# Kernel tuning notes

Measured on AMD Instinct MI355X. Metric: run time of the kernel, lower is better.

The kernel has to match this reference:

```python
import jax, jax.numpy as jnp
import numpy as np

DIM = 1024
NUM_HEADS = 16
HEAD_DIM = DIM // NUM_HEADS
EPS = 1e-5


def layernorm(x, scale, bias):
    # LayerNorm over the last (head_dim) axis
    mu = jnp.mean(x, axis=-1, keepdims=True)
    var = jnp.var(x, axis=-1, keepdims=True)
    return (x - mu) * jax.lax.rsqrt(var + EPS) * scale + bias


def rope(q):
    # q: [B, H, S, Hd]; standard rotate-half RoPE over head_dim
    S, Hd = q.shape[-2], q.shape[-1]
    inv_freq = 1.0 / (10000.0 ** (jnp.arange(0, Hd, 2, dtype=jnp.float32) / Hd))
    ang = jnp.arange(S, dtype=jnp.float32)[:, None] * inv_freq  # [S, Hd/2]
    cos, sin = jnp.cos(ang), jnp.sin(ang)
    q1, q2 = jnp.split(q, 2, axis=-1)
    return jnp.concatenate([q1 * cos - q2 * sin, q1 * sin + q2 * cos], axis=-1)


def setup_inputs() -> dict:
    key = jax.random.key(0)
    ks = jax.random.split(key, 8)
    B, S, S_ctx = 4, 2048, 2048
    s = 0.02
    return {
        "x": jax.random.normal(ks[0], (B, S, DIM), dtype=jnp.float32),
        "context": jax.random.normal(ks[1], (B, S_ctx, DIM), dtype=jnp.float32),
        "q_w": jax.random.normal(ks[2], (DIM, DIM), dtype=jnp.float32) * s,
        "kv_w": jax.random.normal(ks[3], (DIM, 2 * DIM), dtype=jnp.float32) * s,
        "qn_scale": jnp.ones((HEAD_DIM,), jnp.float32),
        "qn_bias": jnp.zeros((HEAD_DIM,), jnp.float32),
        "kn_scale": jnp.ones((HEAD_DIM,), jnp.float32),
        "kn_bias": jnp.zeros((HEAD_DIM,), jnp.float32),
        "proj_w": jax.random.normal(ks[4], (DIM, DIM), dtype=jnp.float32) * s,
        "proj_b": jnp.zeros((DIM,), jnp.float32),
    }


def reference(x, context, q_w, kv_w, qn_scale, qn_bias, kn_scale, kn_bias, proj_w, proj_b):
    B, S, C = x.shape
    S_ctx = context.shape[1]
    H, Hd = NUM_HEADS, HEAD_DIM
    # projections (no bias: qkv_bias=False)
    q = (x @ q_w).reshape(B, S, H, Hd).transpose(0, 2, 1, 3)        # [B,H,S,Hd]
    kv = (context @ kv_w).reshape(B, S_ctx, 2, H, Hd)
    k = kv[:, :, 0].transpose(0, 2, 1, 3)                           # [B,H,Sc,Hd]
    v = kv[:, :, 1].transpose(0, 2, 1, 3)
    # per-head LayerNorm on q and k
    q = layernorm(q, qn_scale, qn_bias)
    k = layernorm(k, kn_scale, kn_bias)
    # RoPE on q only (as in the original forward)
    q = rope(q)
    # SDPA (eval path: no mask, no dropout)
    scale = 1.0 / jnp.sqrt(jnp.float32(Hd))
    logits = jnp.einsum("bhsd,bhtd->bhst", q, k) * scale
    attn = jax.nn.softmax(logits, axis=-1)
    out = jnp.einsum("bhst,bhtd->bhsd", attn, v)                    # [B,H,S,Hd]
    out = out.transpose(0, 2, 1, 3).reshape(B, S, C)
    return out @ proj_w + proj_b
```

## Files before the change

kernel.cpp:

```cpp
#include <hip/hip_runtime.h>
#include <hip/hip_bf16.h>


typedef short bf16x8 __attribute__((ext_vector_type(8)));
typedef float f32x4 __attribute__((ext_vector_type(4)));

__device__ __forceinline__ short f2s(float f) {
    __hip_bfloat16 h = __float2bfloat16(f);
    return __builtin_bit_cast(short, h);
}

__device__ __forceinline__ f32x4 mfma16(bf16x8 a, bf16x8 b, f32x4 c) {
    return __builtin_amdgcn_mfma_f32_16x16x32_bf16(a, b, c, 0, 0, 0);
}

__device__ __forceinline__ void gload16(short* lds, const short* g) {
    __builtin_amdgcn_global_load_lds((const __attribute__((address_space(1))) void*)g,
                                     (__attribute__((address_space(3))) void*)lds,
                                     16, 0, 0);
}

__device__ __forceinline__ void drain_barrier() {
    asm volatile("s_waitcnt vmcnt(0) lgkmcnt(0)" ::: "memory");
    __syncthreads();
}

__device__ __forceinline__ unsigned int fbits(float f) {
    return __builtin_bit_cast(unsigned int, f);
}

__global__ __launch_bounds__(256) void conv_to_bf16(const float* __restrict__ x,
                                                    const float* __restrict__ ctx,
                                                    short* __restrict__ xb,
                                                    short* __restrict__ cb) {
    const size_t NV = 2097152;
    size_t i = (size_t)blockIdx.x * 256 + threadIdx.x;
    const float4* src = (i < NV) ? (const float4*)x : (const float4*)ctx;
    short* dst = (i < NV) ? xb : cb;
    size_t idx = (i < NV) ? i : i - NV;
    float4 v = src[idx];
    short4 o;
    o.x = f2s(v.x); o.y = f2s(v.y); o.z = f2s(v.z); o.w = f2s(v.w);
    ((short4*)dst)[idx] = o;
}

__global__ __launch_bounds__(256) void transpose_weights(
    const float* __restrict__ q_w, const float* __restrict__ kv_w,
    const float* __restrict__ proj_w,
    short* __restrict__ WqT, short* __restrict__ WkvT, short* __restrict__ WpT) {
    __shared__ float t[32][33];
    const float* src; short* dst; int ld, coff;
    switch (blockIdx.z) {
        case 0:  src = q_w;    dst = WqT;                 ld = 1024; coff = 0;    break;
        case 1:  src = kv_w;   dst = WkvT;                ld = 2048; coff = 0;    break;
        case 2:  src = kv_w;   dst = WkvT + 1024 * 1024;  ld = 2048; coff = 1024; break;
        default: src = proj_w; dst = WpT;                 ld = 1024; coff = 0;    break;
    }
    int n0 = blockIdx.x * 32, k0 = blockIdx.y * 32;
    int tx = threadIdx.x & 31, ty = threadIdx.x >> 5;
    #pragma unroll
    for (int j = 0; j < 32; j += 8)
        t[ty + j][tx] = src[(size_t)(k0 + ty + j) * ld + coff + n0 + tx];
    __syncthreads();
    #pragma unroll
    for (int j = 0; j < 32; j += 8)
        dst[(size_t)(n0 + ty + j) * 1024 + k0 + tx] = f2s(t[tx][ty + j]);
}

template <int MODE>
__global__ __launch_bounds__(256) void gemm128(
    const short* __restrict__ A,
    const short* __restrict__ Bt,
    const float* __restrict__ ln_scale,
    const float* __restrict__ ln_bias,
    short* __restrict__ outB,
    short* __restrict__ outB2,
    float* __restrict__ outF,
    const float* __restrict__ bias_vec) {
    __shared__ short smem[24576];
    const int tid = threadIdx.x;
    const int w = tid >> 6, lane = tid & 63, quad = lane >> 4, l15 = lane & 15;
    const int wr = w & 1, wc = w >> 1;
    const int m0 = blockIdx.y * 128, n0 = blockIdx.x * 128;

    const int srow = lane >> 2, slot = lane & 3;
    const int kslot = (slot ^ ((srow >> 1) & 3)) * 8;
    const short* Ag0 = A + (size_t)(m0 + w * 32 + srow) * 1024 + kslot;
    const short* Ag1 = Ag0 + (size_t)16 * 1024;
    const short* Bg0 = Bt + (size_t)(n0 + w * 32 + srow) * 1024 + kslot;
    const short* Bg1 = Bg0 + (size_t)16 * 1024;
    short* Al = smem + w * 1024;
    short* Bl = smem + 4096 + w * 1024;

    f32x4 acc[4][4];
    #pragma unroll
    for (int r = 0; r < 4; r++)
        #pragma unroll
        for (int c = 0; c < 4; c++) acc[r][c] = f32x4{0.f, 0.f, 0.f, 0.f};

    const int rsw = (l15 >> 1) & 3;
    const int rch = (quad ^ rsw) * 8;

    gload16(Al,              Ag0);
    gload16(Al + 512,        Ag1);
    gload16(Bl,              Bg0);
    gload16(Bl + 512,        Bg1);
    gload16(Al + 8192,       Ag0 + 32);
    gload16(Al + 8192 + 512, Ag1 + 32);
    gload16(Bl + 8192,       Bg0 + 32);
    gload16(Bl + 8192 + 512, Bg1 + 32);
    asm volatile("s_waitcnt vmcnt(4) lgkmcnt(0)" ::: "memory");
    __builtin_amdgcn_s_barrier();

    int curo = 0;
    int pfo = 16384;
    #pragma unroll 1
    for (int t = 0; t < 32; t++) {
        if (t < 30) {
            const int k0 = (t + 2) * 32;
            gload16(Al + pfo,       Ag0 + k0);
            gload16(Al + pfo + 512, Ag1 + k0);
            gload16(Bl + pfo,       Bg0 + k0);
            gload16(Bl + pfo + 512, Bg1 + k0);
        }
        bf16x8 af[4], bfr[4];
        #pragma unroll
        for (int rt = 0; rt < 4; rt++)
            af[rt] = *(const bf16x8*)(smem + curo + (wr * 64 + rt * 16 + l15) * 32 + rch);
        #pragma unroll
        for (int ct = 0; ct < 4; ct++)
            bfr[ct] = *(const bf16x8*)(smem + curo + 4096 + (wc * 64 + ct * 16 + l15) * 32 + rch);
        #pragma unroll
        for (int rt = 0; rt < 4; rt++)
            #pragma unroll
            for (int ct = 0; ct < 4; ct++)
                acc[rt][ct] = mfma16(af[rt], bfr[ct], acc[rt][ct]);
        if (t < 30) {
            asm volatile("s_waitcnt vmcnt(4) lgkmcnt(0)" ::: "memory");
        } else {
            asm volatile("s_waitcnt vmcnt(0) lgkmcnt(0)" ::: "memory");
        }
        __builtin_amdgcn_s_barrier();
        curo += 8192; if (curo == 24576) curo = 0;
        pfo  += 8192; if (pfo  == 24576) pfo  = 0;
    }

    const bool vpath = (MODE == 1) && (n0 >= 1024);
    if constexpr (MODE == 0 || MODE == 1) {
        if (!vpath) {
            #pragma unroll
            for (int rt = 0; rt < 4; rt++) {
                #pragma unroll
                for (int i = 0; i < 4; i++) {
                    float s = acc[rt][0][i] + acc[rt][1][i] + acc[rt][2][i] + acc[rt][3][i];
                    float q = acc[rt][0][i] * acc[rt][0][i] + acc[rt][1][i] * acc[rt][1][i] +
                              acc[rt][2][i] * acc[rt][2][i] + acc[rt][3][i] * acc[rt][3][i];
                    #pragma unroll
                    for (int off = 1; off < 16; off <<= 1) {
                        s += __shfl_xor(s, off, 64);
                        q += __shfl_xor(q, off, 64);
                    }
                    float mu = s * (1.f / 64.f);
                    float var = q * (1.f / 64.f) - mu * mu;
                    float rs = rsqrtf(var + 1e-5f);
                    float vals[4];
                    #pragma unroll
                    for (int ct = 0; ct < 4; ct++) {
                        int hd = ct * 16 + l15;
                        vals[ct] = (acc[rt][ct][i] - mu) * rs * ln_scale[hd] + ln_bias[hd];
                    }
                    if constexpr (MODE == 0) {
                        int sp = (m0 + wr * 64 + rt * 16 + quad * 4 + i) & 2047;
                        #pragma unroll
                        for (int ct = 0; ct < 2; ct++) {
                            int hd1 = ct * 16 + l15;
                            float ang = (float)sp * exp2f((float)hd1 * (-13.287712379549449f / 32.f));
                            float sn, cs;
                            sincosf(ang, &sn, &cs);
                            float v1 = vals[ct], v2 = vals[ct + 2];
                            vals[ct]     = v1 * cs - v2 * sn;
                            vals[ct + 2] = v1 * sn + v2 * cs;
                        }
                        #pragma unroll
                        for (int ct = 0; ct < 4; ct++) vals[ct] *= 0.1803368801f;
                    }
                    #pragma unroll
                    for (int ct = 0; ct < 4; ct++) acc[rt][ct][i] = vals[ct];
                }
            }
            drain_barrier();
            short* Csm = smem;
            #pragma unroll
            for (int rt = 0; rt < 4; rt++)
                #pragma unroll
                for (int ct = 0; ct < 4; ct++)
                    #pragma unroll
                    for (int i = 0; i < 4; i++)
                        Csm[(wr * 64 + rt * 16 + quad * 4 + i) * 132 + wc * 64 + ct * 16 + l15] =
                            f2s(acc[rt][ct][i]);
            drain_barrier();
            #pragma unroll
            for (int it = 0; it < 8; it++) {
                int row = it * 16 + (tid >> 4);
                int chunk = tid & 15;
                bf16x8 v = *(const bf16x8*)(Csm + row * 132 + chunk * 8);
                int hh = ((n0 & 1023) >> 6) + (chunk >> 3);
                int m = m0 + row, b = m >> 11, sp = m & 2047;
                *(bf16x8*)(outB + ((size_t)(b * 16 + hh) * 2048 + sp) * 64 + (chunk & 7) * 8) = v;
            }
        } else {
            const int b = m0 >> 11, h = ((n0 - 1024) >> 6) + wc;
            const int sp = (m0 & 2047) + wr * 64 + quad * 4;
            #pragma unroll
            for (int rt = 0; rt < 4; rt++)
                #pragma unroll
                for (int ct = 0; ct < 4; ct++) {
                    short4 pk;
                    pk.x = f2s(acc[rt][ct][0]); pk.y = f2s(acc[rt][ct][1]);
                    pk.z = f2s(acc[rt][ct][2]); pk.w = f2s(acc[rt][ct][3]);
                    int hd = ct * 16 + l15;
                    *(short4*)(outB2 + ((size_t)(b * 16 + h) * 64 + hd) * 2048 + sp + rt * 16) = pk;
                }
        }
    } else {
        #pragma unroll
        for (int rt = 0; rt < 4; rt++)
            #pragma unroll
            for (int i = 0; i < 4; i++) {
                size_t m = m0 + wr * 64 + rt * 16 + quad * 4 + i;
                #pragma unroll
                for (int ct = 0; ct < 4; ct++) {
                    int n = n0 + wc * 64 + ct * 16 + l15;
                    outF[m * 1024 + n] = acc[rt][ct][i] + bias_vec[n];
                }
            }
    }
}

__global__ __launch_bounds__(256, 2) void attn_kernel(
    const short* __restrict__ Q,
    const short* __restrict__ K,
    const short* __restrict__ V,
    short* __restrict__ AO) {
    __shared__ short smem[8192 + 8192 + 2 * 4 * 32 * 72];
    const int tid = threadIdx.x;
    const int w = tid >> 6, lane = tid & 63, quad = lane >> 4, l15 = lane & 15;
    const int bh = blockIdx.x, qt = blockIdx.y;
    const short* Qb = Q + (size_t)bh * 2048 * 64;
    const short* Kb = K + (size_t)bh * 2048 * 64;
    const short* Vb = V + (size_t)bh * 64 * 2048;
    const int q0g[2] = {qt * 128 + w * 32, (qt + 8) * 128 + w * 32};

    const int srow = lane >> 2, slot = lane & 3;
    const int sw = (slot ^ ((srow >> 1) & 3)) * 8;
    const short* Kg = Kb + (size_t)(w * 16 + srow) * 64 + sw;
    const short* Vg = Vb + (size_t)(w * 16 + srow) * 2048 + sw;
    short* Kl0 = smem + w * 512;
    short* Vl0 = smem + 8192 + w * 512;

    bf16x8 bq[2][2][2];
    #pragma unroll
    for (int g = 0; g < 2; g++)
        #pragma unroll
        for (int nt = 0; nt < 2; nt++)
            #pragma unroll
            for (int ks = 0; ks < 2; ks++)
                bq[g][nt][ks] =
                    *(const bf16x8*)(Qb + (size_t)(q0g[g] + nt * 16 + l15) * 64 + ks * 32 + quad * 8);

    f32x4 acco[2][4][2];
    #pragma unroll
    for (int g = 0; g < 2; g++)
        #pragma unroll
        for (int ct = 0; ct < 4; ct++)
            #pragma unroll
            for (int nt = 0; nt < 2; nt++) acco[g][ct][nt] = f32x4{0.f, 0.f, 0.f, 0.f};
    float lsum[2][2] = {{0.f, 0.f}, {0.f, 0.f}};
    const int rsw = (l15 >> 1) & 3;
    const int rch = (quad ^ rsw) * 8;

    gload16(Kl0,        Kg);
    gload16(Kl0 + 2048, Kg + 32);
    gload16(Vl0,        Vg);
    gload16(Vl0 + 2048, Vg + 32);
    drain_barrier();

    #pragma unroll 1
    for (int t = 0; t < 32; t++) {
        const int cur = (t & 1) * 4096;
        if (t < 31) {
            const int nxt = 4096 - cur;
            const int sc = (t + 1) * 64;
            gload16(Kl0 + nxt,        Kg + sc * 64);
            gload16(Kl0 + nxt + 2048, Kg + sc * 64 + 32);
            gload16(Vl0 + nxt,        Vg + sc);
            gload16(Vl0 + nxt + 2048, Vg + sc + 32);
        }
        bf16x8 ak[4][2];
        #pragma unroll
        for (int mt = 0; mt < 4; mt++)
            #pragma unroll
            for (int ks = 0; ks < 2; ks++)
                ak[mt][ks] = *(const bf16x8*)(smem + cur + ks * 2048 + (mt * 16 + l15) * 32 + rch);

        #pragma unroll
        for (int g = 0; g < 2; g++) {
            short* Pw = smem + 16384 + g * 9216 + w * 2304;
            #pragma unroll
            for (int mt = 0; mt < 4; mt++) {
                #pragma unroll
                for (int nt = 0; nt < 2; nt++) {
                    f32x4 st = f32x4{0.f, 0.f, 0.f, 0.f};
                    st = mfma16(ak[mt][0], bq[g][nt][0], st);
                    st = mfma16(ak[mt][1], bq[g][nt][1], st);
                    float e0 = __builtin_amdgcn_exp2f(st[0]);
                    float e1 = __builtin_amdgcn_exp2f(st[1]);
                    float e2 = __builtin_amdgcn_exp2f(st[2]);
                    float e3 = __builtin_amdgcn_exp2f(st[3]);
                    lsum[g][nt] += (e0 + e1) + (e2 + e3);
                    unsigned int p01 = __builtin_amdgcn_perm(fbits(e1), fbits(e0), 0x07060302u);
                    unsigned int p23 = __builtin_amdgcn_perm(fbits(e3), fbits(e2), 0x07060302u);
                    uint2 pw;
                    pw.x = p01; pw.y = p23;
                    *(uint2*)(Pw + (nt * 16 + l15) * 72 + mt * 16 + quad * 4) = pw;
                }
            }
        }
        asm volatile("" ::: "memory");

        bf16x8 av[4][2];
        #pragma unroll
        for (int ct = 0; ct < 4; ct++)
            #pragma unroll
            for (int ks = 0; ks < 2; ks++)
                av[ct][ks] = *(const bf16x8*)(smem + 8192 + cur + ks * 2048 + (ct * 16 + l15) * 32 + rch);

        #pragma unroll
        for (int g = 0; g < 2; g++) {
            short* Pw = smem + 16384 + g * 9216 + w * 2304;
            bf16x8 bp[2][2];
            #pragma unroll
            for (int nt = 0; nt < 2; nt++)
                #pragma unroll
                for (int ks = 0; ks < 2; ks++)
                    bp[nt][ks] = *(const bf16x8*)(Pw + (nt * 16 + l15) * 72 + ks * 32 + quad * 8);
            #pragma unroll
            for (int ct = 0; ct < 4; ct++)
                #pragma unroll
                for (int nt = 0; nt < 2; nt++)
                    #pragma unroll
                    for (int ks = 0; ks < 2; ks++)
                        acco[g][ct][nt] = mfma16(av[ct][ks], bp[nt][ks], acco[g][ct][nt]);
        }
        drain_barrier();
    }

    #pragma unroll
    for (int g = 0; g < 2; g++)
        #pragma unroll
        for (int nt = 0; nt < 2; nt++) {
            lsum[g][nt] += __shfl_xor(lsum[g][nt], 16, 64);
            lsum[g][nt] += __shfl_xor(lsum[g][nt], 32, 64);
        }
    const int b = bh >> 4, h = bh & 15;
    #pragma unroll
    for (int g = 0; g < 2; g++)
        #pragma unroll
        for (int nt = 0; nt < 2; nt++) {
            float inv = 1.f / lsum[g][nt];
            int sq = q0g[g] + nt * 16 + l15;
            #pragma unroll
            for (int ct = 0; ct < 4; ct++) {
                short4 pk;
                pk.x = f2s(acco[g][ct][nt][0] * inv); pk.y = f2s(acco[g][ct][nt][1] * inv);
                pk.z = f2s(acco[g][ct][nt][2] * inv); pk.w = f2s(acco[g][ct][nt][3] * inv);
                *(short4*)(AO + ((size_t)b * 2048 + sq) * 1024 + h * 64 + ct * 16 + quad * 4) = pk;
            }
        }
}

extern "C" void kernel_launch(void* const* d_in, const int* in_sizes, int n_in,
                              void* d_out, int out_size, void* d_ws, size_t ws_size,
                              hipStream_t stream) {
    (void)in_sizes; (void)n_in; (void)out_size; (void)ws_size;
    const float* x      = (const float*)d_in[0];
    const float* ctx    = (const float*)d_in[1];
    const float* q_w    = (const float*)d_in[2];
    const float* kv_w   = (const float*)d_in[3];
    const float* qn_s   = (const float*)d_in[4];
    const float* qn_b   = (const float*)d_in[5];
    const float* kn_s   = (const float*)d_in[6];
    const float* kn_b   = (const float*)d_in[7];
    const float* proj_w = (const float*)d_in[8];
    const float* proj_b = (const float*)d_in[9];
    float* out = (float*)d_out;

    char* ws = (char*)d_ws;
    const size_t MB = 1024 * 1024;
    short* xb   = (short*)(ws + 0 * MB);
    short* cb   = (short*)(ws + 16 * MB);
    short* Qb   = (short*)(ws + 32 * MB);
    short* Kb   = (short*)(ws + 48 * MB);
    short* Vt   = (short*)(ws + 64 * MB);
    short* AO   = (short*)(ws + 80 * MB);
    short* WqT  = (short*)(ws + 96 * MB);
    short* WkvT = (short*)(ws + 98 * MB);
    short* WpT  = (short*)(ws + 102 * MB);

    conv_to_bf16<<<16384, 256, 0, stream>>>(x, ctx, xb, cb);
    transpose_weights<<<dim3(32, 32, 4), 256, 0, stream>>>(q_w, kv_w, proj_w, WqT, WkvT, WpT);
    gemm128<0><<<dim3(8, 64), 256, 0, stream>>>(xb, WqT, qn_s, qn_b, Qb, nullptr, nullptr, nullptr);
    gemm128<1><<<dim3(16, 64), 256, 0, stream>>>(cb, WkvT, kn_s, kn_b, Kb, Vt, nullptr, nullptr);
    attn_kernel<<<dim3(64, 8), 256, 0, stream>>>(Qb, Kb, Vt, AO);
    gemm128<2><<<dim3(8, 64), 256, 0, stream>>>(AO, WpT, nullptr, nullptr, nullptr, nullptr, out, proj_b);
}
```

Measured before the change: 329.6 us.

## Double-buffer GEMM with K=64 stages, swap grid mapping, add occupancy hint

Reworks the GEMM main loop. It moves from a triple-buffered K=32 ring to double-buffered K=64 stages, which halves the number of barrier rounds per K sweep. The grid is transposed so consecutive blocks walk along M while sharing the same weight column tile, which should improve L2 reuse of the B operand. Launch bounds now request two blocks per SM. In exchange, LDS per block grows to 64KB and there are two barriers per iteration, so the prefetch overlaps less with compute.

```diff
diff --git a/kernel.cpp b/kernel.cpp
--- a/kernel.cpp
+++ b/kernel.cpp
@@ -68,7 +68,7 @@
 }
 
 template <int MODE>
-__global__ __launch_bounds__(256) void gemm128(
+__global__ __launch_bounds__(256, 2) void gemm128(
     const short* __restrict__ A,
     const short* __restrict__ Bt,
     const float* __restrict__ ln_scale,
@@ -77,11 +77,11 @@
     short* __restrict__ outB2,
     float* __restrict__ outF,
     const float* __restrict__ bias_vec) {
-    __shared__ short smem[24576];
+    __shared__ short smem[32768];
     const int tid = threadIdx.x;
     const int w = tid >> 6, lane = tid & 63, quad = lane >> 4, l15 = lane & 15;
     const int wr = w & 1, wc = w >> 1;
-    const int m0 = blockIdx.y * 128, n0 = blockIdx.x * 128;
+    const int m0 = blockIdx.x * 128, n0 = blockIdx.y * 128;
 
     const int srow = lane >> 2, slot = lane & 3;
     const int kslot = (slot ^ ((srow >> 1) & 3)) * 8;
@@ -89,8 +89,6 @@
     const short* Ag1 = Ag0 + (size_t)16 * 1024;
     const short* Bg0 = Bt + (size_t)(n0 + w * 32 + srow) * 1024 + kslot;
     const short* Bg1 = Bg0 + (size_t)16 * 1024;
-    short* Al = smem + w * 1024;
-    short* Bl = smem + 4096 + w * 1024;
 
     f32x4 acc[4][4];
     #pragma unroll
@@ -101,48 +99,51 @@
     const int rsw = (l15 >> 1) & 3;
     const int rch = (quad ^ rsw) * 8;
 
-    gload16(Al,              Ag0);
-    gload16(Al + 512,        Ag1);
-    gload16(Bl,              Bg0);
-    gload16(Bl + 512,        Bg1);
-    gload16(Al + 8192,       Ag0 + 32);
-    gload16(Al + 8192 + 512, Ag1 + 32);
-    gload16(Bl + 8192,       Bg0 + 32);
-    gload16(Bl + 8192 + 512, Bg1 + 32);
-    asm volatile("s_waitcnt vmcnt(4) lgkmcnt(0)" ::: "memory");
+    auto stage = [&](int bufo, int kb) {
+        gload16(smem + bufo + w * 1024,               Ag0 + kb);
+        gload16(smem + bufo + w * 1024 + 512,         Ag1 + kb);
+        gload16(smem + bufo + 4096 + w * 1024,        Ag0 + kb + 32);
+        gload16(smem + bufo + 4096 + w * 1024 + 512,  Ag1 + kb + 32);
+        gload16(smem + bufo + 8192 + w * 1024,        Bg0 + kb);
+        gload16(smem + bufo + 8192 + w * 1024 + 512,  Bg1 + kb);
+        gload16(smem + bufo + 12288 + w * 1024,       Bg0 + kb + 32);
+        gload16(smem + bufo + 12288 + w * 1024 + 512, Bg1 + kb + 32);
+    };
+
+    stage(0, 0);
+    stage(16384, 64);
+    asm volatile("s_waitcnt vmcnt(8)" ::: "memory");
     __builtin_amdgcn_s_barrier();
 
-    int curo = 0;
-    int pfo = 16384;
     #pragma unroll 1
-    for (int t = 0; t < 32; t++) {
-        if (t < 30) {
-            const int k0 = (t + 2) * 32;
-            gload16(Al + pfo,       Ag0 + k0);
-            gload16(Al + pfo + 512, Ag1 + k0);
-            gload16(Bl + pfo,       Bg0 + k0);
-            gload16(Bl + pfo + 512, Bg1 + k0);
-        }
-        bf16x8 af[4], bfr[4];
-        #pragma unroll
-        for (int rt = 0; rt < 4; rt++)
-            af[rt] = *(const bf16x8*)(smem + curo + (wr * 64 + rt * 16 + l15) * 32 + rch);
-        #pragma unroll
-        for (int ct = 0; ct < 4; ct++)
-            bfr[ct] = *(const bf16x8*)(smem + curo + 4096 + (wc * 64 + ct * 16 + l15) * 32 + rch);
-        #pragma unroll
-        for (int rt = 0; rt < 4; rt++)
+    for (int t = 0; t < 16; t++) {
+        const int curo = (t & 1) * 16384;
+        #pragma unroll
+        for (int ks = 0; ks < 2; ks++) {
+            bf16x8 af[4], bfr[4];
+            #pragma unroll
+            for (int rt = 0; rt < 4; rt++)
+                af[rt] = *(const bf16x8*)(smem + curo + ks * 4096 +
+                                          (wr * 64 + rt * 16 + l15) * 32 + rch);
             #pragma unroll
             for (int ct = 0; ct < 4; ct++)
-                acc[rt][ct] = mfma16(af[rt], bfr[ct], acc[rt][ct]);
-        if (t < 30) {
-            asm volatile("s_waitcnt vmcnt(4) lgkmcnt(0)" ::: "memory");
+                bfr[ct] = *(const bf16x8*)(smem + curo + 8192 + ks * 4096 +
+                                           (wc * 64 + ct * 16 + l15) * 32 + rch);
+            #pragma unroll
+            for (int rt = 0; rt < 4; rt++)
+                #pragma unroll
+                for (int ct = 0; ct < 4; ct++)
+                    acc[rt][ct] = mfma16(af[rt], bfr[ct], acc[rt][ct]);
+        }
+        asm volatile("s_waitcnt lgkmcnt(0)" ::: "memory");
+        __builtin_amdgcn_s_barrier();
+        if (t < 14) {
+            stage(curo, (t + 2) * 64);
+            asm volatile("s_waitcnt vmcnt(8) lgkmcnt(0)" ::: "memory");
         } else {
             asm volatile("s_waitcnt vmcnt(0) lgkmcnt(0)" ::: "memory");
         }
         __builtin_amdgcn_s_barrier();
-        curo += 8192; if (curo == 24576) curo = 0;
-        pfo  += 8192; if (pfo  == 24576) pfo  = 0;
     }
 
     const bool vpath = (MODE == 1) && (n0 >= 1024);
@@ -409,8 +410,8 @@
 
     conv_to_bf16<<<16384, 256, 0, stream>>>(x, ctx, xb, cb);
     transpose_weights<<<dim3(32, 32, 4), 256, 0, stream>>>(q_w, kv_w, proj_w, WqT, WkvT, WpT);
-    gemm128<0><<<dim3(8, 64), 256, 0, stream>>>(xb, WqT, qn_s, qn_b, Qb, nullptr, nullptr, nullptr);
-    gemm128<1><<<dim3(16, 64), 256, 0, stream>>>(cb, WkvT, kn_s, kn_b, Kb, Vt, nullptr, nullptr);
+    gemm128<0><<<dim3(64, 8), 256, 0, stream>>>(xb, WqT, qn_s, qn_b, Qb, nullptr, nullptr, nullptr);
+    gemm128<1><<<dim3(64, 16), 256, 0, stream>>>(cb, WkvT, kn_s, kn_b, Kb, Vt, nullptr, nullptr);
     attn_kernel<<<dim3(64, 8), 256, 0, stream>>>(Qb, Kb, Vt, AO);
-    gemm128<2><<<dim3(8, 64), 256, 0, stream>>>(AO, WpT, nullptr, nullptr, nullptr, nullptr, out, proj_b);
-}
+    gemm128<2><<<dim3(64, 8), 256, 0, stream>>>(AO, WpT, nullptr, nullptr, nullptr, nullptr, out, proj_b);
+}
```

After: 347.0 us. +5.3%, slower.
